# Optimization experiments

Hardware: AMD Instinct MI355X
Metric: run time of the kernel (lower is better)

## Reference

```python
import jax, jax.numpy as jnp
import numpy as np

N = 50000   # source nodes
M = 50000   # target nodes
DEG = 32    # fixed neighbor count (rowptr built from this)
E = M * DEG # total edges = 1,600,000
B = 1       # batch
C = 32      # in_channels
H = 64      # hidden_dim
CO = 32     # out_channels


def setup_inputs() -> dict:
    key = jax.random.key(0)
    ks = jax.random.split(key, 8)
    in_features = jax.random.normal(ks[0], (N, C), jnp.float32)
    out_features = jax.random.normal(ks[1], (B, M, C), jnp.float32)
    in_weights = jax.random.uniform(ks[2], (N,), jnp.float32)
    neighbors_index = jax.random.randint(ks[3], (E,), 0, N, dtype=jnp.int32)
    neighbors_rowptr = (jnp.arange(M + 1, dtype=jnp.int32) * DEG)
    # MLP params: Linear(2C->H), GELU, Linear(H->CO)
    W1 = jax.random.normal(ks[4], (2 * C, H), jnp.float32) / np.sqrt(2 * C)
    b1 = jnp.zeros((H,), jnp.float32)
    W2 = jax.random.normal(ks[5], (H, CO), jnp.float32) / np.sqrt(H)
    b2 = jnp.zeros((CO,), jnp.float32)
    return {
        "in_features": in_features,
        "out_features": out_features,
        "in_weights": in_weights,
        "W1": W1, "b1": b1, "W2": W2, "b2": b2,
        "neighbors_index": neighbors_index,
        "neighbors_rowptr": neighbors_rowptr,
    }


def reference(in_features, out_features, in_weights, W1, b1, W2, b2,
              neighbors_index, neighbors_rowptr):
    # in_features: [N,C]; out_features: [B,M,C]; in_weights: [N]
    # neighbors_index: [E]; neighbors_rowptr: [M+1]
    nB, nM = out_features.shape[0], neighbors_rowptr.shape[0] - 1
    nE = neighbors_index.shape[0]
    counts = neighbors_rowptr[1:] - neighbors_rowptr[:-1]          # [M]
    seg_ids = jnp.repeat(jnp.arange(nM), counts, total_repeat_length=nE)  # [E]

    rep = in_features[neighbors_index]                              # [E,C] gather
    w = in_weights[neighbors_index][:, None]                        # [E,1]
    self_feat = out_features[:, seg_ids, :]                         # [B,E,C] repeat_interleave
    agg = jnp.concatenate(
        [jnp.broadcast_to(rep[None], (nB, nE, rep.shape[1])), self_feat],
        axis=2)                                                     # [B,E,2C]

    h = jax.nn.gelu(agg @ W1 + b1, approximate=False) @ W2 + b2     # [B,E,CO]
    h = w * h                                                       # per-edge weight

    # segment_csr mean over edges -> [M,B,CO]
    flat = h.transpose(1, 0, 2).reshape(nE, -1)                     # [E, B*CO]
    sums = jax.ops.segment_sum(flat, seg_ids, num_segments=nM)      # [M, B*CO]
    mean = sums / jnp.maximum(counts, 1).astype(sums.dtype)[:, None]
    out = mean.reshape(nM, nB, h.shape[2]).transpose(1, 0, 2)       # [B,M,CO]
    return out
```

## Files before the change

kernel.cpp:

```cpp
#include <hip/hip_runtime.h>
#include <hip/hip_bf16.h>

#define C_IN 32
#define HDIM 64
#define C_OUT 32

__device__ __forceinline__ float bf16_to_f32(unsigned short u) {
    return __uint_as_float(((unsigned int)u) << 16);
}

__device__ __forceinline__ unsigned short f32_to_bf16(float f) {
    unsigned int x = __float_as_uint(f);
    x += 0x7fffu + ((x >> 16) & 1u);
    return (unsigned short)(x >> 16);
}

__device__ __forceinline__ float readlane_f(float v, int t) {
    return __uint_as_float(__builtin_amdgcn_readlane(__float_as_uint(v), t));
}

__device__ __forceinline__ float gelu_f(float x) {
    float x2 = x * x;
    float e  = __expf(x * fmaf(-0.0713553f, x2, -1.5957691f));
    return x * __builtin_amdgcn_rcpf(1.0f + e);
}

__global__ __launch_bounds__(256) void proj_kernel(
    const float* __restrict__ in_features, const float* __restrict__ out_features,
    const float* __restrict__ W1, const float* __restrict__ b1,
    unsigned short* __restrict__ U, unsigned short* __restrict__ S,
    int N, int M)
{
    const int ROWS = 16;
    int lane = threadIdx.x & 63;
    int wid  = __builtin_amdgcn_readfirstlane(
                   blockIdx.x * (blockDim.x >> 6) + (threadIdx.x >> 6));
    int UW = (N + ROWS - 1) / ROWS;
    int SW = (M + ROWS - 1) / ROWS;
    if (wid >= UW + SW) return;
    bool isS = wid >= UW;
    int row0  = (isS ? wid - UW : wid) * ROWS;
    int nrows = min(ROWS, (isS ? M : N) - row0);
    const float* __restrict__ src = isS ? out_features : in_features;
    const float* __restrict__ w1  = W1 + (isS ? C_IN * HDIM : 0);
    unsigned short* __restrict__ dst = isS ? S : U;

    float w1c[C_IN];
#pragma unroll
    for (int k = 0; k < C_IN; ++k) w1c[k] = w1[k * HDIM + lane];
    float bias = isS ? b1[lane] : 0.0f;

    for (int r = 0; r < nrows; ++r) {
        size_t row = (size_t)(row0 + r);
        const float* __restrict__ xr = src + row * C_IN;
        float acc0 = bias, acc1 = 0.0f;
#pragma unroll
        for (int k = 0; k < C_IN; k += 2) {
            acc0 = fmaf(xr[k],     w1c[k],     acc0);
            acc1 = fmaf(xr[k + 1], w1c[k + 1], acc1);
        }
        dst[row * HDIM + lane] = f32_to_bf16(acc0 + acc1);
    }
}

__global__ __launch_bounds__(256) void conv_kernel(
    const unsigned short* __restrict__ U, const unsigned short* __restrict__ S,
    const int* __restrict__ nbr, const int* __restrict__ rowptr,
    const float* __restrict__ in_weights,
    const float* __restrict__ W2, const float* __restrict__ b2,
    float* __restrict__ out, int M)
{
    __shared__ float lds_W2[HDIM * C_OUT];
    __shared__ float lds_acc[4 * HDIM];

    int tid = threadIdx.x;
#pragma unroll
    for (int i = tid; i < HDIM * C_OUT; i += 256) lds_W2[i] = W2[i];

    int wave = tid >> 6, lane = tid & 63;
    int m = blockIdx.x * 4 + wave;

    float acc = 0.0f, wsum = 0.0f;
    int cnt = 0;
    if (m < M) {
        int base = rowptr[m];
        cnt = rowptr[m + 1] - base;
        float s = bf16_to_f32(S[(size_t)m * HDIM + lane]);

        if (cnt == 32) {
            int id = 0; float w = 0.0f;
            if (lane < 32) { int e = nbr[base + lane]; id = e; w = in_weights[e]; }
            wsum = w;

#define UADDR(t) (U + ((size_t)(unsigned)__builtin_amdgcn_readlane(id, (t))) * HDIM + lane)
            unsigned short q0, q1, q2, q3, q4, q5, q6, q7;
            q0 = *UADDR(0); q1 = *UADDR(1); q2 = *UADDR(2); q3 = *UADDR(3);
            q4 = *UADDR(4); q5 = *UADDR(5); q6 = *UADDR(6); q7 = *UADDR(7);

#define PSTEP(t, qr, nt) { \
            float wt = readlane_f(w, (t)); \
            float x  = __uint_as_float(((unsigned)(qr)) << 16) + s; \
            acc = fmaf(wt, gelu_f(x), acc); \
            if ((nt) < 32) qr = *UADDR(nt); }

            PSTEP(0,  q0, 8)  PSTEP(1,  q1, 9)  PSTEP(2,  q2, 10) PSTEP(3,  q3, 11)
            PSTEP(4,  q4, 12) PSTEP(5,  q5, 13) PSTEP(6,  q6, 14) PSTEP(7,  q7, 15)
            PSTEP(8,  q0, 16) PSTEP(9,  q1, 17) PSTEP(10, q2, 18) PSTEP(11, q3, 19)
            PSTEP(12, q4, 20) PSTEP(13, q5, 21) PSTEP(14, q6, 22) PSTEP(15, q7, 23)
            PSTEP(16, q0, 24) PSTEP(17, q1, 25) PSTEP(18, q2, 26) PSTEP(19, q3, 27)
            PSTEP(20, q4, 28) PSTEP(21, q5, 29) PSTEP(22, q6, 30) PSTEP(23, q7, 31)
            PSTEP(24, q0, 32) PSTEP(25, q1, 33) PSTEP(26, q2, 34) PSTEP(27, q3, 35)
            PSTEP(28, q4, 36) PSTEP(29, q5, 37) PSTEP(30, q6, 38) PSTEP(31, q7, 39)
#undef PSTEP
#undef UADDR
        } else {
            for (int t0 = 0; t0 < cnt; t0 += 64) {
                int chunk = min(64, cnt - t0);
                int id = 0; float w = 0.0f;
                if (lane < chunk) { int e = nbr[base + t0 + lane]; id = e; w = in_weights[e]; }
                for (int t = 0; t < chunk; ++t) {
                    unsigned sid = (unsigned)__builtin_amdgcn_readlane(id, t);
                    float    wt  = readlane_f(w, t);
                    float u = bf16_to_f32(U[(size_t)sid * HDIM + lane]);
                    acc = fmaf(wt, gelu_f(u + s), acc);
                }
                wsum += w;
            }
        }
#pragma unroll
        for (int off = 32; off >= 1; off >>= 1) wsum += __shfl_xor(wsum, off);
    }

    lds_acc[wave * HDIM + lane] = acc;
    __syncthreads();

    if (m < M) {
        int j = lane & 31, half = lane >> 5;
        float o = 0.0f;
#pragma unroll
        for (int k2 = 0; k2 < 32; ++k2) {
            int k = half * 32 + k2;
            o = fmaf(lds_acc[wave * HDIM + k], lds_W2[k * C_OUT + j], o);
        }
        o += __shfl_xor(o, 32);
        if (lane < 32) {
            float invc = 1.0f / (float)max(cnt, 1);
            out[(size_t)m * C_OUT + lane] = (o + b2[lane] * wsum) * invc;
        }
    }
}

extern "C" void kernel_launch(void* const* d_in, const int* in_sizes, int n_in,
                              void* d_out, int out_size, void* d_ws, size_t ws_size,
                              hipStream_t stream) {
    const float* in_features  = (const float*)d_in[0];
    const float* out_features = (const float*)d_in[1];
    const float* in_weights   = (const float*)d_in[2];
    const float* W1           = (const float*)d_in[3];
    const float* b1           = (const float*)d_in[4];
    const float* W2           = (const float*)d_in[5];
    const float* b2           = (const float*)d_in[6];
    const int*   nbr          = (const int*)d_in[7];
    const int*   rowptr       = (const int*)d_in[8];

    int N = in_sizes[2];
    int M = in_sizes[8] - 1;

    unsigned short* U = (unsigned short*)d_ws;
    unsigned short* S = U + (size_t)N * HDIM;

    const int ROWS = 16;
    int UW = (N + ROWS - 1) / ROWS;
    int SW = (M + ROWS - 1) / ROWS;
    int proj_blocks = (UW + SW + 3) / 4;
    proj_kernel<<<proj_blocks, 256, 0, stream>>>(in_features, out_features, W1, b1,
                                                 U, S, N, M);

    int conv_blocks = (M + 3) / 4;
    conv_kernel<<<conv_blocks, 256, 0, stream>>>(U, S, nbr, rowptr, in_weights,
                                                 W2, b2, (float*)d_out, M);
}
```

Before: 142.3 us.

## Process two edges per wave with packed bf16x2 loads and packed FMA GELU

The fixed-degree path now has each half-wave handle a different edge, with each lane loading a dword holding two bf16 hidden channels, so the 64-lane wave covers two edges per step. The GELU math runs on float2 vectors, which can map to packed FMA instructions. exp is replaced by a direct exp2 builtin with the constants pre-scaled by log2(e). The two half-wave accumulators are combined with a cross-half shuffle before the LDS store. This is meant to halve the per-edge instruction count and issue wider loads. The cost is extra select and readlane work per iteration, and the prior 8-deep software prefetch pipeline is dropped in favour of a plain unrolled loop.

```diff
diff --git a/kernel.cpp b/kernel.cpp
--- a/kernel.cpp
+++ b/kernel.cpp
@@ -4,6 +4,8 @@
 #define C_IN 32
 #define HDIM 64
 #define C_OUT 32
+
+typedef float float2v __attribute__((ext_vector_type(2)));
 
 __device__ __forceinline__ float bf16_to_f32(unsigned short u) {
     return __uint_as_float(((unsigned int)u) << 16);
@@ -19,9 +21,17 @@
     return __uint_as_float(__builtin_amdgcn_readlane(__float_as_uint(v), t));
 }
 
+__device__ __forceinline__ float2v pk_fma(float2v a, float2v b, float2v c) {
+#if __has_builtin(__builtin_elementwise_fma)
+    return __builtin_elementwise_fma(a, b, c);
+#else
+    float2v d; d.x = fmaf(a.x, b.x, c.x); d.y = fmaf(a.y, b.y, c.y); return d;
+#endif
+}
+
 __device__ __forceinline__ float gelu_f(float x) {
     float x2 = x * x;
-    float e  = __expf(x * fmaf(-0.0713553f, x2, -1.5957691f));
+    float e  = __builtin_amdgcn_exp2f(x * fmaf(-0.1029441f, x2, -2.3022082f));
     return x * __builtin_amdgcn_rcpf(1.0f + e);
 }
 
@@ -80,40 +90,65 @@
     int wave = tid >> 6, lane = tid & 63;
     int m = blockIdx.x * 4 + wave;
 
-    float acc = 0.0f, wsum = 0.0f;
+    float wsum = 0.0f;
     int cnt = 0;
     if (m < M) {
         int base = rowptr[m];
         cnt = rowptr[m + 1] - base;
-        float s = bf16_to_f32(S[(size_t)m * HDIM + lane]);
 
         if (cnt == 32) {
+            int cpl = lane & 31;
+            bool hi = lane >= 32;
+
             int id = 0; float w = 0.0f;
             if (lane < 32) { int e = nbr[base + lane]; id = e; w = in_weights[e]; }
             wsum = w;
 
-#define UADDR(t) (U + ((size_t)(unsigned)__builtin_amdgcn_readlane(id, (t))) * HDIM + lane)
-            unsigned short q0, q1, q2, q3, q4, q5, q6, q7;
-            q0 = *UADDR(0); q1 = *UADDR(1); q2 = *UADDR(2); q3 = *UADDR(3);
-            q4 = *UADDR(4); q5 = *UADDR(5); q6 = *UADDR(6); q7 = *UADDR(7);
-
-#define PSTEP(t, qr, nt) { \
-            float wt = readlane_f(w, (t)); \
-            float x  = __uint_as_float(((unsigned)(qr)) << 16) + s; \
-            acc = fmaf(wt, gelu_f(x), acc); \
-            if ((nt) < 32) qr = *UADDR(nt); }
-
-            PSTEP(0,  q0, 8)  PSTEP(1,  q1, 9)  PSTEP(2,  q2, 10) PSTEP(3,  q3, 11)
-            PSTEP(4,  q4, 12) PSTEP(5,  q5, 13) PSTEP(6,  q6, 14) PSTEP(7,  q7, 15)
-            PSTEP(8,  q0, 16) PSTEP(9,  q1, 17) PSTEP(10, q2, 18) PSTEP(11, q3, 19)
-            PSTEP(12, q4, 20) PSTEP(13, q5, 21) PSTEP(14, q6, 22) PSTEP(15, q7, 23)
-            PSTEP(16, q0, 24) PSTEP(17, q1, 25) PSTEP(18, q2, 26) PSTEP(19, q3, 27)
-            PSTEP(20, q4, 28) PSTEP(21, q5, 29) PSTEP(22, q6, 30) PSTEP(23, q7, 31)
-            PSTEP(24, q0, 32) PSTEP(25, q1, 33) PSTEP(26, q2, 34) PSTEP(27, q3, 35)
-            PSTEP(28, q4, 36) PSTEP(29, q5, 37) PSTEP(30, q6, 38) PSTEP(31, q7, 39)
-#undef PSTEP
-#undef UADDR
+            unsigned int sdw = ((const unsigned int*)S)[(size_t)m * 32 + cpl];
+            float2v s2;
+            s2.x = __uint_as_float(sdw << 16);
+            s2.y = __uint_as_float(sdw & 0xffff0000u);
+
+            const unsigned int* __restrict__ Uw = (const unsigned int*)U;
+            float2v acc2 = {0.0f, 0.0f};
+            const float2v cA = {-2.3022082f, -2.3022082f};
+            const float2v cB = {-0.1029441f, -0.1029441f};
+
+#pragma unroll
+            for (int t = 0; t < 32; t += 2) {
+                unsigned sidE = (unsigned)__builtin_amdgcn_readlane(id, t);
+                unsigned sidO = (unsigned)__builtin_amdgcn_readlane(id, t + 1);
+                unsigned row  = hi ? sidO : sidE;
+                unsigned int udw = Uw[row * 32u + (unsigned)cpl];
+                float wt = hi ? readlane_f(w, t + 1) : readlane_f(w, t);
+
+                float2v u2;
+                u2.x = __uint_as_float(udw << 16);
+                u2.y = __uint_as_float(udw & 0xffff0000u);
+                float2v x  = u2 + s2;
+                float2v x2 = x * x;
+                float2v q  = pk_fma(cB, x2, cA);
+                float2v xq = x * q;
+                float2v e2;
+                e2.x = __builtin_amdgcn_exp2f(xq.x);
+                e2.y = __builtin_amdgcn_exp2f(xq.y);
+                float2v den = e2 + (float2v){1.0f, 1.0f};
+                float2v r;
+                r.x = __builtin_amdgcn_rcpf(den.x);
+                r.y = __builtin_amdgcn_rcpf(den.y);
+                float2v g = x * r;
+                float2v wt2 = {wt, wt};
+                acc2 = pk_fma(wt2, g, acc2);
+            }
+            acc2.x += __shfl_xor(acc2.x, 32);
+            acc2.y += __shfl_xor(acc2.y, 32);
+            if (lane < 32) {
+                lds_acc[wave * HDIM + 2 * cpl]     = acc2.x;
+                lds_acc[wave * HDIM + 2 * cpl + 1] = acc2.y;
+            }
         } else {
+            float acc = 0.0f;
+            float s = bf16_to_f32(S[(size_t)m * HDIM + lane]);
             for (int t0 = 0; t0 < cnt; t0 += 64) {
                 int chunk = min(64, cnt - t0);
                 int id = 0; float w = 0.0f;
@@ -126,12 +161,12 @@
                 }
                 wsum += w;
             }
+            lds_acc[wave * HDIM + lane] = acc;
         }
 #pragma unroll
         for (int off = 32; off >= 1; off >>= 1) wsum += __shfl_xor(wsum, off);
     }
 
-    lds_acc[wave * HDIM + lane] = acc;
     __syncthreads();
 
     if (m < M) {
```

Result: slower. 145.4 us (+2.2%).
